# Kernel tuning notes

Measured on AMD Instinct MI355X. Metric: run time of the kernel, lower is better.

## Reference

```python
import jax, jax.numpy as jnp
import numpy as np

B, T, E, V = 2048, 256, 124, 65
LN_EPS = 1e-5


def setup_inputs() -> dict:
    key = jax.random.key(0)
    ks = jax.random.split(key, 16)
    s = 0.02
    return {
        "idx": jax.random.randint(ks[0], (B, T), 0, V),
        "token_emb": jax.random.normal(ks[1], (V, E), jnp.float32) * s,
        "pos_emb": jax.random.normal(ks[2], (T, E), jnp.float32) * s,
        "w_ih": jax.random.normal(ks[3], (3 * E, 2 * E), jnp.float32) * s,
        "w_hh": jax.random.normal(ks[4], (3 * E, E), jnp.float32) * s,
        "b_ih": jnp.zeros((3 * E,), jnp.float32),
        "b_hh": jnp.zeros((3 * E,), jnp.float32),
        "w_p": jax.random.normal(ks[5], (1, E), jnp.float32) * s,
        "b_p": jnp.zeros((1,), jnp.float32),
        "w_m": jax.random.normal(ks[6], (E, E), jnp.float32) * s,
        "b_m": jnp.zeros((E,), jnp.float32),
        "ln_g": jnp.ones((E,), jnp.float32),
        "ln_b": jnp.zeros((E,), jnp.float32),
        "w_head": jax.random.normal(ks[7], (V, E), jnp.float32) * s,
        "b_head": jnp.zeros((V,), jnp.float32),
    }


def reference(idx, token_emb, pos_emb, w_ih, w_hh, b_ih, b_hh,
              w_p, b_p, w_m, b_m, ln_g, ln_b, w_head, b_head):
    Bb, Tt = idx.shape
    e = token_emb.shape[1]
    # embeddings (dropout in eval mode = identity)
    x = token_emb[idx] + pos_emb[None, :Tt, :]  # [B,T,E]

    def step(carry, x_t):
        h, m = carry
        comb = jnp.concatenate([x_t, m], axis=1)            # [B,2E]
        gi = comb @ w_ih.T + b_ih                            # [B,3E]
        gh = h @ w_hh.T + b_hh                               # [B,3E]
        ir, iz, i_n = jnp.split(gi, 3, axis=1)               # PyTorch gate order r,z,n
        hr, hz, h_n = jnp.split(gh, 3, axis=1)
        r = jax.nn.sigmoid(ir + hr)
        z = jax.nn.sigmoid(iz + hz)
        n = jnp.tanh(i_n + r * h_n)
        h_new = (1.0 - z) * n + z * h
        p = jax.nn.sigmoid(h_new @ w_p.T + b_p)              # [B,1]
        cand = jnp.tanh(h_new @ w_m.T + b_m)                 # [B,E]
        m_new = (1.0 - p) * m + p * cand
        return (h_new, m_new), h_new

    h0 = jnp.zeros((Bb, e), x.dtype)
    m0 = jnp.zeros((Bb, e), x.dtype)
    _, hs = jax.lax.scan(step, (h0, m0), jnp.swapaxes(x, 0, 1))  # hs: [T,B,E]
    rnn_out = jnp.swapaxes(hs, 0, 1)                              # [B,T,E]

    mu = jnp.mean(rnn_out, axis=-1, keepdims=True)
    var = jnp.mean((rnn_out - mu) ** 2, axis=-1, keepdims=True)
    y = (rnn_out - mu) * jax.lax.rsqrt(var + LN_EPS) * ln_g + ln_b

    logits = y @ w_head.T + b_head                                # [B,T,V]
    return logits
```

## Files before the change

kernel.cpp:

```cpp
#include <hip/hip_runtime.h>
#include <math.h>

#define B_   2048
#define T_   256
#define E_   124
#define V_   65
#define E2_  248
#define R_   8
#define NT_  512
#define NB_  (B_ / R_)
#define NKC  4
#define TCH  8

#define WS_WX  0
#define WS_WM2 49152
#define WS_HH  98304
#define WS_WM  147456
#define WS_HD  163840
#define WS_END 174080

#define HSTR 136
#define GXSTR 376
#define L_M   0
#define L_H   2176
#define L_ZR  4352
#define L_GX  4624
#define L_XE  52752
#define L_BRZ 70160
#define L_BIN 71152
#define L_BHN 71648
#define L_BM  72144
#define L_WP  72640
#define L_C1  73136
#define L_C2B 73408
#define L_IDX 73680
#define SMEM_BYTES 81872

typedef __attribute__((ext_vector_type(8))) short short8v;
typedef __attribute__((ext_vector_type(4))) float float4v;

__device__ __forceinline__ unsigned short f2bf(float x) {
    unsigned u = __float_as_uint(x);
    unsigned r = (u + 0x7fffu + ((u >> 16) & 1u)) >> 16;
    return (unsigned short)r;
}
__device__ __forceinline__ float bf2f(unsigned short s) {
    return __uint_as_float(((unsigned)s) << 16);
}
__device__ __forceinline__ float sigmoid_f(float x) {
    return 1.0f / (1.0f + __expf(-x));
}
__device__ __forceinline__ float tanh_f(float x) {
    return 2.0f / (1.0f + __expf(-2.0f * x)) - 1.0f;
}

__global__ void prep_weights(const float* __restrict__ w_ih,
                             const float* __restrict__ w_hh,
                             const float* __restrict__ w_m,
                             const float* __restrict__ w_head,
                             const float* __restrict__ ln_g,
                             unsigned short* __restrict__ ws) {
    for (int n = blockIdx.x * blockDim.x + threadIdx.x; n < WS_END;
         n += gridDim.x * blockDim.x) {
        const int r9 = n & 511;
        const int lane = r9 >> 3, j = r9 & 7;
        const int krel = (lane >> 4) * 8 + j;
        const int colrel = lane & 15;
        float w = 0.f;
        if (n < WS_WM2) {
            const int blk = n >> 9;
            const int c = blk & 3, tt = (blk >> 2) & 7, g = blk >> 5;
            const int k = c * 32 + krel, e = tt * 16 + colrel;
            if (k < E_ && e < E_) w = w_ih[(g * E_ + e) * E2_ + k];
        } else if (n < WS_WM) {
            if (n < WS_HH) {
                const int blk = (n - WS_WM2) >> 9;
                const int c = blk & 3, tt = (blk >> 2) & 7, g = blk >> 5;
                const int k = c * 32 + krel, e = tt * 16 + colrel;
                if (k < E_ && e < E_) w = w_ih[(g * E_ + e) * E2_ + E_ + k];
            } else {
                const int blk = (n - WS_HH) >> 9;
                const int c = blk & 3, tt = (blk >> 2) & 7, g = blk >> 5;
                const int k = c * 32 + krel, e = tt * 16 + colrel;
                if (k < E_ && e < E_) w = w_hh[(g * E_ + e) * E_ + k];
            }
        } else if (n < WS_HD) {
            const int blk = (n - WS_WM) >> 9;
            const int c = blk & 3, tt = blk >> 2;
            const int k = c * 32 + krel, e = tt * 16 + colrel;
            if (k < E_ && e < E_) w = w_m[e * E_ + k];
        } else {
            const int blk = (n - WS_HD) >> 9;
            const int c = blk & 3, tt = blk >> 2;
            const int k = c * 32 + krel, v = tt * 16 + colrel;
            if (k < E_ && v < V_) w = w_head[v * E_ + k] * ln_g[k];
        }
        ws[n] = f2bf(w);
    }
}

__global__ void __launch_bounds__(NT_, 2)
gru_main(const int* __restrict__ idx, const float* __restrict__ tok,
         const float* __restrict__ pos,
         const float* __restrict__ b_ih, const float* __restrict__ b_hh,
         const float* __restrict__ w_p, const float* __restrict__ b_p,
         const float* __restrict__ b_m,
         const float* __restrict__ ln_g, const float* __restrict__ ln_b,
         const float* __restrict__ w_head, const float* __restrict__ b_head,
         const unsigned short* __restrict__ ws, float* __restrict__ out) {
    extern __shared__ char smraw[];
    unsigned short* Ms = (unsigned short*)(smraw + L_M);
    unsigned short* Hs = (unsigned short*)(smraw + L_H);
    unsigned short* ZRs = (unsigned short*)(smraw + L_ZR);
    unsigned short* GXs = (unsigned short*)(smraw + L_GX);
    unsigned short* XEs = (unsigned short*)(smraw + L_XE);
    float* BRZs = (float*)(smraw + L_BRZ);
    float* BINs = (float*)(smraw + L_BIN);
    float* BHNs = (float*)(smraw + L_BHN);
    float* BMs = (float*)(smraw + L_BM);
    float* WPs = (float*)(smraw + L_WP);
    float* C1s = (float*)(smraw + L_C1);
    float* C2Bs = (float*)(smraw + L_C2B);
    int* IDXs = (int*)(smraw + L_IDX);

    const int tid = threadIdx.x;
    const int lane = tid & 63;
    const int wv = tid >> 6;
    const int b0 = blockIdx.x * R_;
    const int frow = lane & 15;
    const int fgrp = lane >> 4;
    const int eo = wv * 16 + frow;
    const bool eon = (eo < E_);
    const bool actx = (fgrp < 2) && eon;
    const bool hdw = (wv >= 2) && (wv < 7);
    const int vo = (wv - 2) * 16 + frow;
    const int rb = (fgrp < 2) ? fgrp * 4 : (fgrp - 2) * 4 + 2;

    for (int i = tid; i < E2_; i += NT_) BRZs[i] = b_ih[i] + b_hh[i];
    for (int i = tid; i < E_; i += NT_) {
        BINs[i] = b_ih[E2_ + i];
        BHNs[i] = b_hh[E2_ + i];
        BMs[i] = b_m[i];
        WPs[i] = w_p[i];
    }
    for (int v = tid; v < V_; v += NT_) {
        float s1 = 0.f, s2 = 0.f;
        for (int e = 0; e < E_; ++e) {
            const float w = w_head[v * E_ + e];
            s1 += ln_g[e] * w;
            s2 += ln_b[e] * w;
        }
        C1s[v] = s1;
        C2Bs[v] = s2 + b_head[v];
    }
    for (int i = tid; i < R_ * T_; i += NT_) IDXs[i] = idx[b0 * T_ + i];
    for (int i = tid; i < 2312; i += NT_) ((unsigned short*)smraw)[i] = 0;
    for (int i = tid; i < TCH * R_ * HSTR; i += NT_) XEs[i] = 0;
    const float bp = b_p[0];

    short8v hhf[3][NKC], wm2f[3][NKC], wmf[NKC], hdf[NKC], wpf[NKC];
#pragma unroll
    for (int g = 0; g < 3; ++g)
#pragma unroll
        for (int c = 0; c < NKC; ++c) {
            hhf[g][c]  = *(const short8v*)&ws[WS_HH  + ((g * 8 + wv) * NKC + c) * 512 + lane * 8];
            wm2f[g][c] = *(const short8v*)&ws[WS_WM2 + ((g * 8 + wv) * NKC + c) * 512 + lane * 8];
        }
    {
        const int ht = hdw ? (wv - 2) : 0;
#pragma unroll
        for (int c = 0; c < NKC; ++c) {
            wmf[c] = *(const short8v*)&ws[WS_WM + (wv * NKC + c) * 512 + lane * 8];
            hdf[c] = *(const short8v*)&ws[WS_HD + (ht * NKC + c) * 512 + lane * 8];
        }
    }
#pragma unroll
    for (int c = 0; c < NKC; ++c) {
#pragma unroll
        for (int j = 0; j < 8; ++j) {
            const int k = c * 32 + fgrp * 8 + j;
            float v = 0.f;
            if (k < E_) v = (frow < 8) ? w_p[k] : (1.0f / (float)E_);
            wpf[c][j] = (short)f2bf(v);
        }
    }

    const unsigned short* Mrow = (frow < 8) ? Ms + frow * HSTR : ZRs;
    const unsigned short* Hrow = (frow < 8) ? Hs + frow * HSTR : ZRs;
    const unsigned short* Xrow = (frow < 8) ? XEs + frow * HSTR : ZRs;
    const int xstep = (frow < 8) ? R_ * HSTR : 0;
    __syncthreads();

    float ghc[3][2] = {{0.f, 0.f}, {0.f, 0.f}, {0.f, 0.f}};
    float hprev[2] = {0.f, 0.f};
    float mprev[2] = {0.f, 0.f};

    for (int t = 0; t < T_; ++t) {
        if ((t & 7) == 0) {
#pragma unroll
            for (int p = 0; p < 4; ++p) {
                const int i = tid + p * NT_;
                if (i < TCH * R_ * 31) {
                    const int mt = i / 248;
                    const int rem = i - mt * 248;
                    const int rr = rem / 31, q = rem - (rem / 31) * 31;
                    const int token = IDXs[rr * T_ + t + mt];
                    const int k = q * 4;
                    const float4 tv = *(const float4*)&tok[token * E_ + k];
                    const float4 pv = *(const float4*)&pos[(t + mt) * E_ + k];
#pragma unroll
                    for (int jj = 0; jj < 4; ++jj) {
                        const float x = ((const float*)&tv)[jj] + ((const float*)&pv)[jj];
                        XEs[(mt * R_ + rr) * HSTR + k + jj] = f2bf(x);
                    }
                }
            }
            __syncthreads();
#pragma unroll
            for (int g = 0; g < 3; ++g) {
                short8v bx[NKC];
#pragma unroll
                for (int c = 0; c < NKC; ++c)
                    bx[c] = *(const short8v*)&ws[WS_WX + ((g * 8 + wv) * NKC + c) * 512 + lane * 8];
                for (int mt = 0; mt < TCH; ++mt) {
                    float4v ax = (float4v){0.f, 0.f, 0.f, 0.f};
#pragma unroll
                    for (int c = 0; c < NKC; ++c) {
                        const short8v a = *(const short8v*)&Xrow[mt * xstep + c * 32 + fgrp * 8];
                        ax = __builtin_amdgcn_mfma_f32_16x16x32_bf16(a, bx[c], ax, 0, 0, 0);
                    }
                    if (actx) {
#pragma unroll
                        for (int j = 0; j < 4; ++j)
                            GXs[(mt * R_ + fgrp * 4 + j) * GXSTR + g * E_ + eo] = f2bf(ax[j]);
                    }
                }
            }
        }

        {
            float gx[2][3];
#pragma unroll
            for (int jj = 0; jj < 2; ++jj) {
                const unsigned short* gxp = &GXs[((t & 7) * R_ + rb + jj) * GXSTR];
                gx[jj][0] = bf2f(gxp[eo]);
                gx[jj][1] = bf2f(gxp[E_ + eo]);
                gx[jj][2] = bf2f(gxp[E2_ + eo]);
            }
            short8v am[NKC];
#pragma unroll
            for (int c = 0; c < NKC; ++c)
                am[c] = *(const short8v*)&Mrow[c * 32 + fgrp * 8];
            float4v accm[3];
#pragma unroll
            for (int g = 0; g < 3; ++g) accm[g] = (float4v){0.f, 0.f, 0.f, 0.f};
#pragma unroll
            for (int g = 0; g < 3; ++g)
#pragma unroll
                for (int c = 0; c < NKC; ++c)
                    accm[g] = __builtin_amdgcn_mfma_f32_16x16x32_bf16(am[c], wm2f[g][c], accm[g], 0, 0, 0);
            float am2[3][2];
#pragma unroll
            for (int g = 0; g < 3; ++g) {
                const float tm2 = __shfl_xor(accm[g][2], 32);
                const float tm3 = __shfl_xor(accm[g][3], 32);
                am2[g][0] = (fgrp < 2) ? accm[g][0] : tm2;
                am2[g][1] = (fgrp < 2) ? accm[g][1] : tm3;
            }
            if (eon) {
                const float brz0 = BRZs[eo], brz1 = BRZs[E_ + eo];
                const float bin = BINs[eo], bhn = BHNs[eo];
#pragma unroll
                for (int jj = 0; jj < 2; ++jj) {
                    const int r = rb + jj;
                    const float rg = sigmoid_f(gx[jj][0] + am2[0][jj] + ghc[0][jj] + brz0);
                    const float z = sigmoid_f(gx[jj][1] + am2[1][jj] + ghc[1][jj] + brz1);
                    const float nn = tanh_f(gx[jj][2] + am2[2][jj] + bin + rg * (ghc[2][jj] + bhn));
                    const float hv = (1.0f - z) * nn + z * hprev[jj];
                    const unsigned short h1 = f2bf(hv);
                    hprev[jj] = bf2f(h1);
                    Hs[r * HSTR + eo] = h1;
                }
            }
        }
        __syncthreads();

        {
            short8v ahw[NKC];
#pragma unroll
            for (int c = 0; c < NKC; ++c)
                ahw[c] = *(const short8v*)&Hrow[c * 32 + fgrp * 8];

            float4v cc = (float4v){0.f, 0.f, 0.f, 0.f};
            float4v pm = (float4v){0.f, 0.f, 0.f, 0.f};
            float4v gr = (float4v){0.f, 0.f, 0.f, 0.f};
            float4v agh[3];
#pragma unroll
            for (int g = 0; g < 3; ++g) agh[g] = (float4v){0.f, 0.f, 0.f, 0.f};
#pragma unroll
            for (int c = 0; c < NKC; ++c) {
                cc = __builtin_amdgcn_mfma_f32_16x16x32_bf16(ahw[c], wmf[c], cc, 0, 0, 0);
                pm = __builtin_amdgcn_mfma_f32_16x16x32_bf16(ahw[c], wpf[c], pm, 0, 0, 0);
                gr = __builtin_amdgcn_mfma_f32_16x16x32_bf16(ahw[c], ahw[c], gr, 0, 0, 0);
#pragma unroll
                for (int g = 0; g < 3; ++g)
                    agh[g] = __builtin_amdgcn_mfma_f32_16x16x32_bf16(ahw[c], hhf[g][c], agh[g], 0, 0, 0);
            }
            float4v ad = (float4v){0.f, 0.f, 0.f, 0.f};
            if (hdw) {
#pragma unroll
                for (int c = 0; c < NKC; ++c)
                    ad = __builtin_amdgcn_mfma_f32_16x16x32_bf16(ahw[c], hdf[c], ad, 0, 0, 0);
            }

#pragma unroll
            for (int g = 0; g < 3; ++g) {
                const float tg2 = __shfl_xor(agh[g][2], 32);
                const float tg3 = __shfl_xor(agh[g][3], 32);
                ghc[g][0] = (fgrp < 2) ? agh[g][0] : tg2;
                ghc[g][1] = (fgrp < 2) ? agh[g][1] : tg3;
            }

            const float tc2 = __shfl_xor(cc[2], 32), tc3 = __shfl_xor(cc[3], 32);
            const float tp2 = __shfl_xor(pm[2], 32), tp3 = __shfl_xor(pm[3], 32);
            const float ta2 = __shfl_xor(ad[2], 32), ta3 = __shfl_xor(ad[3], 32);
            float ccl[2], pml[2], adl[2], s2l[2];
            ccl[0] = (fgrp < 2) ? cc[0] : tc2;
            ccl[1] = (fgrp < 2) ? cc[1] : tc3;
            pml[0] = (fgrp < 2) ? pm[0] : tp2;
            pml[1] = (fgrp < 2) ? pm[1] : tp3;
            adl[0] = (fgrp < 2) ? ad[0] : ta2;
            adl[1] = (fgrp < 2) ? ad[1] : ta3;
            {
                const float d0a = __shfl(gr[0], 20 * (fgrp & 1) + 0);
                const float d1a = __shfl(gr[1], 20 * (fgrp & 1) + 1);
                const float d0b = __shfl(gr[2], 20 * (fgrp & 1) + 2);
                const float d1b = __shfl(gr[3], 20 * (fgrp & 1) + 3);
                s2l[0] = (fgrp < 2) ? d0a : d0b;
                s2l[1] = (fgrp < 2) ? d1a : d1b;
            }

            const float bm = BMs[eon ? eo : 0];
            const float c1v = C1s[(hdw && vo < V_) ? vo : 0];
            const float c2v = C2Bs[(hdw && vo < V_) ? vo : 0];
#pragma unroll
            for (int jj = 0; jj < 2; ++jj) {
                const int r = rb + jj;
                const float other = __shfl_xor(pml[jj], 8);
                const float pdot = (frow < 8) ? pml[jj] : other;
                const float mu = (frow < 8) ? other : pml[jj];
                const float pv = sigmoid_f(pdot + bp);
                const float var = s2l[jj] * (1.0f / (float)E_) - mu * mu;
                const float rs = rsqrtf(var + 1e-5f);
                if (eon) {
                    const float cand = tanh_f(ccl[jj] + bm);
                    const float mnew = (1.0f - pv) * mprev[jj] + pv * cand;
                    const unsigned short m1 = f2bf(mnew);
                    mprev[jj] = bf2f(m1);
                    Ms[r * HSTR + eo] = m1;
                }
                if (hdw && vo < V_) {
                    const float lg = rs * (adl[jj] - mu * c1v) + c2v;
                    __builtin_nontemporal_store(
                        lg, &out[((size_t)(b0 + r) * T_ + t) * V_ + vo]);
                }
            }
        }
        __syncthreads();
    }
}

extern "C" void kernel_launch(void* const* d_in, const int* in_sizes, int n_in,
                              void* d_out, int out_size, void* d_ws, size_t ws_size,
                              hipStream_t stream) {
    const int* idx = (const int*)d_in[0];
    const float* tok = (const float*)d_in[1];
    const float* pos = (const float*)d_in[2];
    const float* w_ih = (const float*)d_in[3];
    const float* w_hh = (const float*)d_in[4];
    const float* b_ih = (const float*)d_in[5];
    const float* b_hh = (const float*)d_in[6];
    const float* w_p = (const float*)d_in[7];
    const float* b_p = (const float*)d_in[8];
    const float* w_m = (const float*)d_in[9];
    const float* b_m = (const float*)d_in[10];
    const float* ln_g = (const float*)d_in[11];
    const float* ln_b = (const float*)d_in[12];
    const float* w_head = (const float*)d_in[13];
    const float* b_head = (const float*)d_in[14];
    float* out = (float*)d_out;
    unsigned short* ws = (unsigned short*)d_ws;

    prep_weights<<<680, 256, 0, stream>>>(w_ih, w_hh, w_m, w_head, ln_g, ws);

    (void)hipFuncSetAttribute((const void*)gru_main,
                              hipFuncAttributeMaxDynamicSharedMemorySize,
                              SMEM_BYTES);
    gru_main<<<NB_, NT_, SMEM_BYTES, stream>>>(idx, tok, pos, b_ih, b_hh, w_p, b_p,
                                               b_m, ln_g, ln_b, w_head, b_head, ws, out);
}
```

Before: 684.3 us.

## Defer head projection by one step with double-buffered hidden state

Double-buffers the hidden-state shared tile and moves the LayerNorm/head MFMA and logit store for step t-1 into phase one of step t, running them alongside the gate computation. This takes the head projection off the post-sync critical path of the recurrence. The loop runs one extra iteration to drain the last step, and LN statistics are carried in registers across the iteration. It costs a little more shared memory and an extra loop iteration.

```diff
diff --git a/kernel.cpp b/kernel.cpp
--- a/kernel.cpp
+++ b/kernel.cpp
@@ -22,19 +22,19 @@
 #define HSTR 136
 #define GXSTR 376
 #define L_M   0
-#define L_H   2176
-#define L_ZR  4352
-#define L_GX  4624
-#define L_XE  52752
-#define L_BRZ 70160
-#define L_BIN 71152
-#define L_BHN 71648
-#define L_BM  72144
-#define L_WP  72640
-#define L_C1  73136
-#define L_C2B 73408
-#define L_IDX 73680
-#define SMEM_BYTES 81872
+#define L_HA  2176
+#define L_HB  4352
+#define L_ZR  6528
+#define L_GX  6800
+#define L_XE  54928
+#define L_BRZ 72336
+#define L_BIN 73328
+#define L_BHN 73824
+#define L_BM  74320
+#define L_C1  74816
+#define L_C2B 75088
+#define L_IDX 75360
+#define SMEM_BYTES 83552
 
 typedef __attribute__((ext_vector_type(8))) short short8v;
 typedef __attribute__((ext_vector_type(4))) float float4v;
@@ -110,7 +110,6 @@
          const unsigned short* __restrict__ ws, float* __restrict__ out) {
     extern __shared__ char smraw[];
     unsigned short* Ms = (unsigned short*)(smraw + L_M);
-    unsigned short* Hs = (unsigned short*)(smraw + L_H);
     unsigned short* ZRs = (unsigned short*)(smraw + L_ZR);
     unsigned short* GXs = (unsigned short*)(smraw + L_GX);
     unsigned short* XEs = (unsigned short*)(smraw + L_XE);
@@ -118,7 +117,6 @@
     float* BINs = (float*)(smraw + L_BIN);
     float* BHNs = (float*)(smraw + L_BHN);
     float* BMs = (float*)(smraw + L_BM);
-    float* WPs = (float*)(smraw + L_WP);
     float* C1s = (float*)(smraw + L_C1);
     float* C2Bs = (float*)(smraw + L_C2B);
     int* IDXs = (int*)(smraw + L_IDX);
@@ -141,7 +139,6 @@
         BINs[i] = b_ih[E2_ + i];
         BHNs[i] = b_hh[E2_ + i];
         BMs[i] = b_m[i];
-        WPs[i] = w_p[i];
     }
     for (int v = tid; v < V_; v += NT_) {
         float s1 = 0.f, s2 = 0.f;
@@ -154,7 +151,7 @@
         C2Bs[v] = s2 + b_head[v];
     }
     for (int i = tid; i < R_ * T_; i += NT_) IDXs[i] = idx[b0 * T_ + i];
-    for (int i = tid; i < 2312; i += NT_) ((unsigned short*)smraw)[i] = 0;
+    for (int i = tid; i < 3400; i += NT_) ((unsigned short*)smraw)[i] = 0;
     for (int i = tid; i < TCH * R_ * HSTR; i += NT_) XEs[i] = 0;
     const float bp = b_p[0];
 
@@ -186,7 +183,6 @@
     }
 
     const unsigned short* Mrow = (frow < 8) ? Ms + frow * HSTR : ZRs;
-    const unsigned short* Hrow = (frow < 8) ? Hs + frow * HSTR : ZRs;
     const unsigned short* Xrow = (frow < 8) ? XEs + frow * HSTR : ZRs;
     const int xstep = (frow < 8) ? R_ * HSTR : 0;
     __syncthreads();
@@ -194,9 +190,16 @@
     float ghc[3][2] = {{0.f, 0.f}, {0.f, 0.f}, {0.f, 0.f}};
     float hprev[2] = {0.f, 0.f};
     float mprev[2] = {0.f, 0.f};
-
-    for (int t = 0; t < T_; ++t) {
-        if ((t & 7) == 0) {
+    float mul[2] = {0.f, 0.f};
+    float rsl[2] = {1.f, 1.f};
+
+    for (int t = 0; t <= T_; ++t) {
+        unsigned short* Hw = (unsigned short*)(smraw + ((t & 1) ? L_HB : L_HA));
+        const unsigned short* HrB = (const unsigned short*)(smraw + ((t & 1) ? L_HA : L_HB));
+        const unsigned short* Hrowprev = (frow < 8) ? HrB + frow * HSTR : ZRs;
+        const unsigned short* Hrowcur = (frow < 8) ? (const unsigned short*)Hw + frow * HSTR : ZRs;
+
+        if (t < T_ && (t & 7) == 0) {
 #pragma unroll
             for (int p = 0; p < 4; ++p) {
                 const int i = tid + p * NT_;
@@ -239,57 +242,82 @@
         }
 
         {
-            float gx[2][3];
-#pragma unroll
-            for (int jj = 0; jj < 2; ++jj) {
-                const unsigned short* gxp = &GXs[((t & 7) * R_ + rb + jj) * GXSTR];
-                gx[jj][0] = bf2f(gxp[eo]);
-                gx[jj][1] = bf2f(gxp[E_ + eo]);
-                gx[jj][2] = bf2f(gxp[E2_ + eo]);
-            }
-            short8v am[NKC];
-#pragma unroll
-            for (int c = 0; c < NKC; ++c)
-                am[c] = *(const short8v*)&Mrow[c * 32 + fgrp * 8];
-            float4v accm[3];
-#pragma unroll
-            for (int g = 0; g < 3; ++g) accm[g] = (float4v){0.f, 0.f, 0.f, 0.f};
-#pragma unroll
-            for (int g = 0; g < 3; ++g)
+            float4v ad = (float4v){0.f, 0.f, 0.f, 0.f};
+            if (t > 0 && hdw) {
+#pragma unroll
+                for (int c = 0; c < NKC; ++c) {
+                    const short8v ahp = *(const short8v*)&Hrowprev[c * 32 + fgrp * 8];
+                    ad = __builtin_amdgcn_mfma_f32_16x16x32_bf16(ahp, hdf[c], ad, 0, 0, 0);
+                }
+            }
+            if (t < T_) {
+                float gx[2][3];
+#pragma unroll
+                for (int jj = 0; jj < 2; ++jj) {
+                    const unsigned short* gxp = &GXs[((t & 7) * R_ + rb + jj) * GXSTR];
+                    gx[jj][0] = bf2f(gxp[eo]);
+                    gx[jj][1] = bf2f(gxp[E_ + eo]);
+                    gx[jj][2] = bf2f(gxp[E2_ + eo]);
+                }
+                short8v am[NKC];
 #pragma unroll
                 for (int c = 0; c < NKC; ++c)
-                    accm[g] = __builtin_amdgcn_mfma_f32_16x16x32_bf16(am[c], wm2f[g][c], accm[g], 0, 0, 0);
-            float am2[3][2];
-#pragma unroll
-            for (int g = 0; g < 3; ++g) {
-                const float tm2 = __shfl_xor(accm[g][2], 32);
-                const float tm3 = __shfl_xor(accm[g][3], 32);
-                am2[g][0] = (fgrp < 2) ? accm[g][0] : tm2;
-                am2[g][1] = (fgrp < 2) ? accm[g][1] : tm3;
-            }
-            if (eon) {
-                const float brz0 = BRZs[eo], brz1 = BRZs[E_ + eo];
-                const float bin = BINs[eo], bhn = BHNs[eo];
-#pragma unroll
-                for (int jj = 0; jj < 2; ++jj) {
-                    const int r = rb + jj;
-                    const float rg = sigmoid_f(gx[jj][0] + am2[0][jj] + ghc[0][jj] + brz0);
-                    const float z = sigmoid_f(gx[jj][1] + am2[1][jj] + ghc[1][jj] + brz1);
-                    const float nn = tanh_f(gx[jj][2] + am2[2][jj] + bin + rg * (ghc[2][jj] + bhn));
-                    const float hv = (1.0f - z) * nn + z * hprev[jj];
-                    const unsigned short h1 = f2bf(hv);
-                    hprev[jj] = bf2f(h1);
-                    Hs[r * HSTR + eo] = h1;
-                }
-            }
-        }
+                    am[c] = *(const short8v*)&Mrow[c * 32 + fgrp * 8];
+                float4v accm[3];
+#pragma unroll
+                for (int g = 0; g < 3; ++g) accm[g] = (float4v){0.f, 0.f, 0.f, 0.f};
+#pragma unroll
+                for (int g = 0; g < 3; ++g)
+#pragma unroll
+                    for (int c = 0; c < NKC; ++c)
+                        accm[g] = __builtin_amdgcn_mfma_f32_16x16x32_bf16(am[c], wm2f[g][c], accm[g], 0, 0, 0);
+                float am2[3][2];
+#pragma unroll
+                for (int g = 0; g < 3; ++g) {
+                    const float tm2 = __shfl_xor(accm[g][2], 32);
+                    const float tm3 = __shfl_xor(accm[g][3], 32);
+                    am2[g][0] = (fgrp < 2) ? accm[g][0] : tm2;
+                    am2[g][1] = (fgrp < 2) ? accm[g][1] : tm3;
+                }
+                if (eon) {
+                    const float brz0 = BRZs[eo], brz1 = BRZs[E_ + eo];
+                    const float bin = BINs[eo], bhn = BHNs[eo];
+#pragma unroll
+                    for (int jj = 0; jj < 2; ++jj) {
+                        const int r = rb + jj;
+                        const float rg = sigmoid_f(gx[jj][0] + am2[0][jj] + ghc[0][jj] + brz0);
+                        const float z = sigmoid_f(gx[jj][1] + am2[1][jj] + ghc[1][jj] + brz1);
+                        const float nn = tanh_f(gx[jj][2] + am2[2][jj] + bin + rg * (ghc[2][jj] + bhn));
+                        const float hv = (1.0f - z) * nn + z * hprev[jj];
+                        const unsigned short h1 = f2bf(hv);
+                        hprev[jj] = bf2f(h1);
+                        Hw[r * HSTR + eo] = h1;
+                    }
+                }
+            }
+            if (t > 0 && hdw) {
+                const float ta2 = __shfl_xor(ad[2], 32), ta3 = __shfl_xor(ad[3], 32);
+                const float adl0 = (fgrp < 2) ? ad[0] : ta2;
+                const float adl1 = (fgrp < 2) ? ad[1] : ta3;
+                if (vo < V_) {
+                    const float c1v = C1s[vo], c2v = C2Bs[vo];
+                    __builtin_nontemporal_store(
+                        rsl[0] * (adl0 - mul[0] * c1v) + c2v,
+                        &out[((size_t)(b0 + rb + 0) * T_ + (t - 1)) * V_ + vo]);
+                    __builtin_nontemporal_store(
+                        rsl[1] * (adl1 - mul[1] * c1v) + c2v,
+                        &out[((size_t)(b0 + rb + 1) * T_ + (t - 1)) * V_ + vo]);
+                }
+            }
+        }
+        if (t == T_) break;
         __syncthreads();
 
         {
             short8v ahw[NKC];
 #pragma unroll
             for (int c = 0; c < NKC; ++c)
-                ahw[c] = *(const short8v*)&Hrow[c * 32 + fgrp * 8];
+                ahw[c] = *(const short8v*)&Hrowcur[c * 32 + fgrp * 8];
 
             float4v cc = (float4v){0.f, 0.f, 0.f, 0.f};
             float4v pm = (float4v){0.f, 0.f, 0.f, 0.f};
@@ -305,12 +333,6 @@
 #pragma unroll
                 for (int g = 0; g < 3; ++g)
                     agh[g] = __builtin_amdgcn_mfma_f32_16x16x32_bf16(ahw[c], hhf[g][c], agh[g], 0, 0, 0);
-            }
-            float4v ad = (float4v){0.f, 0.f, 0.f, 0.f};
-            if (hdw) {
-#pragma unroll
-                for (int c = 0; c < NKC; ++c)
-                    ad = __builtin_amdgcn_mfma_f32_16x16x32_bf16(ahw[c], hdf[c], ad, 0, 0, 0);
             }
 
 #pragma unroll
@@ -323,14 +345,11 @@
 
             const float tc2 = __shfl_xor(cc[2], 32), tc3 = __shfl_xor(cc[3], 32);
             const float tp2 = __shfl_xor(pm[2], 32), tp3 = __shfl_xor(pm[3], 32);
-            const float ta2 = __shfl_xor(ad[2], 32), ta3 = __shfl_xor(ad[3], 32);
-            float ccl[2], pml[2], adl[2], s2l[2];
+            float ccl[2], pml[2], s2l[2];
             ccl[0] = (fgrp < 2) ? cc[0] : tc2;
             ccl[1] = (fgrp < 2) ? cc[1] : tc3;
             pml[0] = (fgrp < 2) ? pm[0] : tp2;
             pml[1] = (fgrp < 2) ? pm[1] : tp3;
-            adl[0] = (fgrp < 2) ? ad[0] : ta2;
-            adl[1] = (fgrp < 2) ? ad[1] : ta3;
             {
                 const float d0a = __shfl(gr[0], 20 * (fgrp & 1) + 0);
                 const float d1a = __shfl(gr[1], 20 * (fgrp & 1) + 1);
@@ -341,8 +360,6 @@
             }
 
             const float bm = BMs[eon ? eo : 0];
-            const float c1v = C1s[(hdw && vo < V_) ? vo : 0];
-            const float c2v = C2Bs[(hdw && vo < V_) ? vo : 0];
 #pragma unroll
             for (int jj = 0; jj < 2; ++jj) {
                 const int r = rb + jj;
@@ -352,17 +369,14 @@
                 const float pv = sigmoid_f(pdot + bp);
                 const float var = s2l[jj] * (1.0f / (float)E_) - mu * mu;
                 const float rs = rsqrtf(var + 1e-5f);
+                mul[jj] = mu;
+                rsl[jj] = rs;
                 if (eon) {
                     const float cand = tanh_f(ccl[jj] + bm);
                     const float mnew = (1.0f - pv) * mprev[jj] + pv * cand;
                     const unsigned short m1 = f2bf(mnew);
                     mprev[jj] = bf2f(m1);
                     Ms[r * HSTR + eo] = m1;
-                }
-                if (hdw && vo < V_) {
-                    const float lg = rs * (adl[jj] - mu * c1v) + c2v;
-                    __builtin_nontemporal_store(
-                        lg, &out[((size_t)(b0 + r) * T_ + t) * V_ + vo]);
                 }
             }
         }
```

Result: slower. 745.6 us (+9.0%).
